# Performance work log

Hardware: AMD Instinct MI355X
Metric: run time of the kernel (lower is better)

Reference implementation:

```python
import jax, jax.numpy as jnp
import numpy as np

N = 100000   # nodes
E = 1250000  # edges
IN = 64
HID = 64
OUT = 64


def setup_inputs() -> dict:
    key = jax.random.key(0)
    ks = jax.random.split(key, 8)
    x = jax.random.normal(ks[0], (N, IN), dtype=jnp.float32)
    edge_index = jax.random.randint(ks[1], (2, E), 0, N, dtype=jnp.int64)
    s_in = 1.0 / np.sqrt(IN)
    s_h = 1.0 / np.sqrt(HID)
    W1 = jax.random.normal(ks[2], (IN, HID), dtype=jnp.float32) * s_in
    b1 = jnp.zeros((HID,), dtype=jnp.float32)
    W2 = jax.random.normal(ks[3], (HID, HID), dtype=jnp.float32) * s_h
    b2 = jnp.zeros((HID,), dtype=jnp.float32)
    Wp = jax.random.normal(ks[4], (HID, OUT), dtype=jnp.float32) * s_h
    bp = jnp.zeros((OUT,), dtype=jnp.float32)
    return {"x": x, "edge_index": edge_index, "W1": W1, "b1": b1,
            "W2": W2, "b2": b2, "Wp": Wp, "bp": bp}


def _gcn_conv(h, W, b, src, dst, inv_sqrt_deg):
    # PyG GCNConv with add_self_loops: x' = D^{-1/2} (A+I) D^{-1/2} (h W) + b
    m = h @ W                                   # [N, F]
    norm = inv_sqrt_deg[src] * inv_sqrt_deg[dst]  # [E]
    agg = jax.ops.segment_sum(m[src] * norm[:, None], dst, num_segments=N)
    agg = agg + m * (inv_sqrt_deg * inv_sqrt_deg)[:, None]  # self-loop term (norm = 1/deg)
    return agg + b


def reference(x, edge_index, W1, b1, W2, b2, Wp, bp):
    src = edge_index[0]
    dst = edge_index[1]
    # degree with self-loops (edge weight 1)
    deg = jax.ops.segment_sum(jnp.ones((E,), dtype=x.dtype), dst, num_segments=N) + 1.0
    inv_sqrt_deg = jax.lax.rsqrt(deg)
    # dropout is identity in eval mode
    h = jax.nn.relu(_gcn_conv(x, W1, b1, src, dst, inv_sqrt_deg))
    h = jax.nn.relu(_gcn_conv(h, W2, b2, src, dst, inv_sqrt_deg))
    z = h @ Wp + bp                             # [N, OUT]
    return z
```

## Files before the change

kernel.cpp:

```cpp
#include <hip/hip_runtime.h>

#define F 64
#define NPART 256
#define CAP 8192

typedef unsigned short u16x8 __attribute__((ext_vector_type(8)));
typedef _Float16       f16x8 __attribute__((ext_vector_type(8)));
typedef float          f32x4 __attribute__((ext_vector_type(4)));

__device__ __forceinline__ float h2f(unsigned short u) {
    _Float16 h; __builtin_memcpy(&h, &u, 2); return (float)h;
}
__device__ __forceinline__ unsigned short f2h(float f) {
    _Float16 h = (_Float16)f; unsigned short u; __builtin_memcpy(&u, &h, 2); return u;
}


__global__ void k_binit(int* bbase) {
    bbase[threadIdx.x * 16] = threadIdx.x * CAP;
}

template<int EPT>
__global__ __launch_bounds__(256)
void k_binGemm1(const int* __restrict__ src, const int* __restrict__ dst,
                int* bbase, int2* staging,
                const float* __restrict__ x, const float* __restrict__ W1,
                unsigned short* __restrict__ mhA,
                int nE, int nN, int nBin, int nTiles)
{
    __shared__ int lcnt[NPART];
    __shared__ int lbase[NPART];
    __shared__ _Float16 Wt[64 * 72];
    const int t = threadIdx.x;

    if (blockIdx.x < nBin) {
        const int i0 = blockIdx.x * 256 * EPT;
        lcnt[t] = 0;
        __syncthreads();
        int es[EPT], ed[EPT], bk[EPT];
#pragma unroll
        for (int k = 0; k < EPT; ++k) {
            const int i = i0 + k * 256 + t;
            if (i < nE) {
                es[k] = src[i];
                ed[k] = dst[i];
                bk[k] = (int)(((long long)ed[k] * NPART) / nN);
                atomicAdd(&lcnt[bk[k]], 1);
            } else bk[k] = -1;
        }
        __syncthreads();
        lbase[t] = atomicAdd(&bbase[t * 16], lcnt[t]);
        lcnt[t] = 0;
        __syncthreads();
#pragma unroll
        for (int k = 0; k < EPT; ++k) {
            if (bk[k] >= 0) {
                const int r   = atomicAdd(&lcnt[bk[k]], 1);
                const int pos = lbase[bk[k]] + r;
                if (pos < (bk[k] + 1) * CAP)
                    staging[pos] = make_int2(es[k], ed[k]);
            }
        }
    } else {
#pragma unroll
        for (int i = 0; i < 16; ++i) {
            const int idx = i * 256 + t;
            Wt[(idx & 63) * 72 + (idx >> 6)] = (_Float16)W1[idx];
        }
        __syncthreads();
        const int w    = t >> 6;
        const int l    = t & 63;
        const int lr   = l & 15;
        const int lg   = l >> 4;
        const int tile = (blockIdx.x - nBin) * 4 + w;
        if (tile >= nTiles) return;

        f16x8 bf[2][4];
#pragma unroll
        for (int kt = 0; kt < 2; ++kt)
#pragma unroll
            for (int ct = 0; ct < 4; ++ct)
                bf[kt][ct] = *(const f16x8*)&Wt[(ct * 16 + lr) * 72 + kt * 32 + lg * 8];

        const float* rp = x + (size_t)(tile * 16 + lr) * F;
        f16x8 af[2];
#pragma unroll
        for (int kt = 0; kt < 2; ++kt) {
            const float4 v0 = *(const float4*)(rp + kt * 32 + lg * 8);
            const float4 v1 = *(const float4*)(rp + kt * 32 + lg * 8 + 4);
            f16x8 a;
            a[0] = (_Float16)v0.x; a[1] = (_Float16)v0.y;
            a[2] = (_Float16)v0.z; a[3] = (_Float16)v0.w;
            a[4] = (_Float16)v1.x; a[5] = (_Float16)v1.y;
            a[6] = (_Float16)v1.z; a[7] = (_Float16)v1.w;
            af[kt] = a;
        }

        f32x4 acc[4] = {{0.f,0.f,0.f,0.f},{0.f,0.f,0.f,0.f},{0.f,0.f,0.f,0.f},{0.f,0.f,0.f,0.f}};
#pragma unroll
        for (int kt = 0; kt < 2; ++kt)
#pragma unroll
            for (int ct = 0; ct < 4; ++ct)
                acc[ct] = __builtin_amdgcn_mfma_f32_16x16x32_f16(af[kt], bf[kt][ct], acc[ct], 0, 0, 0);

        const int rowb = tile * 16 + lg * 4;
#pragma unroll
        for (int ct = 0; ct < 4; ++ct) {
            const int c = ct * 16 + lr;
#pragma unroll
            for (int r = 0; r < 4; ++r)
                mhA[(size_t)(rowb + r) * F + c] = f2h(acc[ct][r]);
        }
    }
}

__global__ __launch_bounds__(256)
void k_sortP(const int2* __restrict__ staging, const int* __restrict__ bbase,
             int* __restrict__ ebs, int* __restrict__ rowptr,
             float* __restrict__ isd, unsigned short* __restrict__ mhA,
             int nN, int nE) {
    __shared__ int pc[NPART];
    __shared__ int pcv[NPART];
    __shared__ int cnt[512];
    __shared__ int cur[512];
    const int p = blockIdx.x;
    const int t = threadIdx.x;

    int cval = bbase[t * 16] - t * CAP;
    if (cval > CAP) cval = CAP;
    if (cval < 0)   cval = 0;
    pc[t]  = cval;
    pcv[t] = cval;
    __syncthreads();
#pragma unroll
    for (int off = 1; off < NPART; off <<= 1) {
        const int a = (t >= off) ? pc[t - off] : 0;
        __syncthreads();
        pc[t] += a;
        __syncthreads();
    }
    const int cg    = pcv[p];
    const int ebase = pc[p] - cg;
    const int lo    = (int)(((long long)nN * p + NPART - 1) / NPART);
    const int hi    = (int)(((long long)nN * (p + 1) + NPART - 1) / NPART);
    const int npn   = hi - lo;

    cnt[t] = 0; cnt[t + 256] = 0;
    __syncthreads();
    const int2* st = staging + (size_t)p * CAP;
    for (int j = t; j < cg; j += 256) atomicAdd(&cnt[st[j].y - lo], 1);
    __syncthreads();

    const int c0 = cnt[t], c1 = cnt[t + 256];
#pragma unroll
    for (int off = 1; off < 512; off <<= 1) {
        const int a0 = (t >= off) ? cnt[t - off] : 0;
        const int a1 = (t + 256 >= off) ? cnt[t + 256 - off] : 0;
        __syncthreads();
        cnt[t] += a0; cnt[t + 256] += a1;
        __syncthreads();
    }
    const int e0 = cnt[t] - c0, e1 = cnt[t + 256] - c1;
    cur[t] = e0; cur[t + 256] = e1;

    if (t < npn)        { rowptr[lo + t]        = ebase + e0; isd[lo + t]        = rsqrtf((float)c0 + 1.0f); }
    if (t + 256 < npn)  { rowptr[lo + t + 256]  = ebase + e1; isd[lo + t + 256]  = rsqrtf((float)c1 + 1.0f); }
    if (p == NPART - 1 && t == 0) rowptr[nN] = ebase + cg;
    __syncthreads();

    for (int j = t; j < cg; j += 256) {
        const int2 e = st[j];
        const int  r = atomicAdd(&cur[e.y - lo], 1);
        ebs[ebase + r] = e.x;
    }

    for (int r = t; r < npn; r += 256) {
        const int row = lo + r;
        const float s = rsqrtf((float)((r < 256 ? c0 : 0) + 0) + 1.0f);
        (void)s;
        const float sr = isd[row];
        u16x8* rp = (u16x8*)(mhA + (size_t)row * F);
#pragma unroll
        for (int q = 0; q < 8; ++q) {
            u16x8 v = rp[q];
            u16x8 o;
#pragma unroll
            for (int j = 0; j < 8; ++j) o[j] = f2h(h2f(v[j]) * sr);
            rp[q] = o;
        }
    }
}


template<bool PROJ>
__global__ __launch_bounds__(256)
void k_aggGemm(const unsigned short* __restrict__ mhIn,
               const float* __restrict__ isd,
               const int* __restrict__ rowptr, const int* __restrict__ ebs,
               const float* __restrict__ W, const float* __restrict__ bin,
               const float* __restrict__ bout,
               unsigned short* __restrict__ outh, float* __restrict__ outf,
               int nN)
{
    __shared__ _Float16 Wt[64 * 72];
    __shared__ _Float16 A[32 * 72];
    const int t = threadIdx.x;
#pragma unroll
    for (int i = 0; i < 16; ++i) {
        const int idx = i * 256 + t;
        Wt[(idx & 63) * 72 + (idx >> 6)] = (_Float16)W[idx];
    }

    const int w  = t >> 6;
    const int l  = t & 63;
    const int nb = blockIdx.x * 32;
    const float bl = bin[l];

#pragma unroll
    for (int i = 0; i < 8; ++i) {
        const int n = nb + w * 8 + i;
        const int beg = __builtin_amdgcn_readfirstlane(rowptr[n]);
        const int end = __builtin_amdgcn_readfirstlane(rowptr[n + 1]);
        const float di = isd[n];
        float a0 = h2f(mhIn[(size_t)n * F + l]);
        float a1 = 0.f, a2 = 0.f, a3 = 0.f;
        int e = beg;
        for (; e + 8 <= end; e += 8) {
            const int s0 = ebs[e + 0], s1 = ebs[e + 1], s2 = ebs[e + 2], s3 = ebs[e + 3];
            const int s4 = ebs[e + 4], s5 = ebs[e + 5], s6 = ebs[e + 6], s7 = ebs[e + 7];
            const float v0 = h2f(mhIn[(size_t)s0 * F + l]);
            const float v1 = h2f(mhIn[(size_t)s1 * F + l]);
            const float v2 = h2f(mhIn[(size_t)s2 * F + l]);
            const float v3 = h2f(mhIn[(size_t)s3 * F + l]);
            const float v4 = h2f(mhIn[(size_t)s4 * F + l]);
            const float v5 = h2f(mhIn[(size_t)s5 * F + l]);
            const float v6 = h2f(mhIn[(size_t)s6 * F + l]);
            const float v7 = h2f(mhIn[(size_t)s7 * F + l]);
            a0 += v0; a1 += v1; a2 += v2; a3 += v3;
            a0 += v4; a1 += v5; a2 += v6; a3 += v7;
        }
        for (; e + 2 <= end; e += 2) {
            const int s0 = ebs[e + 0], s1 = ebs[e + 1];
            a0 += h2f(mhIn[(size_t)s0 * F + l]);
            a1 += h2f(mhIn[(size_t)s1 * F + l]);
        }
        if (e < end) a2 += h2f(mhIn[(size_t)ebs[e] * F + l]);
        const float v = ((a0 + a1) + (a2 + a3)) * di;
        A[(w * 8 + i) * 72 + l] = (_Float16)fmaxf(v + bl, 0.f);
    }
    __syncthreads();

    const int lr = l & 15;
    const int lg = l >> 4;
    const int th = w >> 1;
    const int ch = (w & 1) * 2;

    f16x8 bf[2][2];
#pragma unroll
    for (int kt = 0; kt < 2; ++kt)
#pragma unroll
        for (int ct = 0; ct < 2; ++ct)
            bf[kt][ct] = *(const f16x8*)&Wt[((ch + ct) * 16 + lr) * 72 + kt * 32 + lg * 8];

    f16x8 af[2];
#pragma unroll
    for (int kt = 0; kt < 2; ++kt)
        af[kt] = *(const f16x8*)&A[(th * 16 + lr) * 72 + kt * 32 + lg * 8];

    f32x4 acc[2] = {{0.f,0.f,0.f,0.f},{0.f,0.f,0.f,0.f}};
#pragma unroll
    for (int kt = 0; kt < 2; ++kt)
#pragma unroll
        for (int ct = 0; ct < 2; ++ct)
            acc[ct] = __builtin_amdgcn_mfma_f32_16x16x32_f16(af[kt], bf[kt][ct], acc[ct], 0, 0, 0);

    const int rowb = nb + th * 16 + lg * 4;
    float4 sc4;
    if (!PROJ) sc4 = *(const float4*)&isd[rowb];
    const float scv[4] = {sc4.x, sc4.y, sc4.z, sc4.w};
#pragma unroll
    for (int ct = 0; ct < 2; ++ct) {
        const int c = (ch + ct) * 16 + lr;
        float badd = 0.f;
        if (PROJ) badd = bout[c];
#pragma unroll
        for (int r = 0; r < 4; ++r) {
            if (PROJ) outf[(size_t)(rowb + r) * F + c] = acc[ct][r] + badd;
            else      outh[(size_t)(rowb + r) * F + c] = f2h(acc[ct][r] * scv[r]);
        }
    }
}


extern "C" void kernel_launch(void* const* d_in, const int* in_sizes, int n_in,
                              void* d_out, int out_size, void* d_ws, size_t ws_size,
                              hipStream_t stream)
{
    const float* x   = (const float*)d_in[0];
    const int*   ei  = (const int*)d_in[1];
    const float* W1  = (const float*)d_in[2];
    const float* b1  = (const float*)d_in[3];
    const float* W2  = (const float*)d_in[4];
    const float* b2  = (const float*)d_in[5];
    const float* Wp  = (const float*)d_in[6];
    const float* bp  = (const float*)d_in[7];
    float*       z   = (float*)d_out;

    const int nN = in_sizes[0] / F;
    const int nE = in_sizes[1] / 2;
    const int* srcp = ei;
    const int* dstp = ei + nE;

    char* ws = (char*)d_ws;
    size_t o = 0;
    auto alloc = [&](size_t bytes) { char* p = ws + o; o += (bytes + 255) & ~(size_t)255; return p; };
    float* isd    = (float*)alloc((size_t)nN * 4);
    int*   rowptr = (int*)  alloc(((size_t)nN + 1) * 4);
    int*   bbase  = (int*)  alloc((size_t)NPART * 16 * 4);
    int*   ebs    = (int*)  alloc((size_t)nE * 4);
    char*  U      = alloc((size_t)NPART * CAP * 8);
    int2*  staging = (int2*)U;
    unsigned short* mhB = (unsigned short*)U;
    unsigned short* mhA = (unsigned short*)alloc((size_t)nN * F * 2);

    constexpr int EPT = 16;
    const int gbB    = (nE + 256 * EPT - 1) / (256 * EPT);
    const int nTiles = nN / 16;
    const int gbG    = (nTiles + 3) / 4;
    const int gbF    = (nN + 31) / 32;

    k_binit<<<1, NPART, 0, stream>>>(bbase);
    k_binGemm1<EPT><<<gbB + gbG, 256, 0, stream>>>(srcp, dstp, bbase, staging,
                                                   x, W1, mhA, nE, nN, gbB, nTiles);
    k_sortP<<<NPART, 256, 0, stream>>>(staging, bbase, ebs, rowptr, isd, mhA, nN, nE);

    k_aggGemm<false><<<gbF, 256, 0, stream>>>(mhA, isd, rowptr, ebs, W2, b1, nullptr,
                                              mhB, nullptr, nN);
    k_aggGemm<true><<<gbF, 256, 0, stream>>>(mhB, isd, rowptr, ebs, Wp, b2, bp,
                                             nullptr, z, nN);
}
```

Before: 129.6 us.

## Split each wavefront across four edges with 8-byte vector gathers in aggregation

```diff
diff --git a/kernel.cpp b/kernel.cpp
--- a/kernel.cpp
+++ b/kernel.cpp
@@ -5,7 +5,9 @@
 #define CAP 8192
 
 typedef unsigned short u16x8 __attribute__((ext_vector_type(8)));
+typedef unsigned short u16x4 __attribute__((ext_vector_type(4)));
 typedef _Float16       f16x8 __attribute__((ext_vector_type(8)));
+typedef _Float16       f16x4 __attribute__((ext_vector_type(4)));
 typedef float          f32x4 __attribute__((ext_vector_type(4)));
 
 __device__ __forceinline__ float h2f(unsigned short u) {
@@ -176,8 +178,6 @@
 
     for (int r = t; r < npn; r += 256) {
         const int row = lo + r;
-        const float s = rsqrtf((float)((r < 256 ? c0 : 0) + 0) + 1.0f);
-        (void)s;
         const float sr = isd[row];
         u16x8* rp = (u16x8*)(mhA + (size_t)row * F);
 #pragma unroll
@@ -213,8 +213,10 @@
 
     const int w  = t >> 6;
     const int l  = t & 63;
+    const int q  = l >> 4;
+    const int r  = l & 15;
     const int nb = blockIdx.x * 32;
-    const float bl = bin[l];
+    const float4 bb = *(const float4*)(bin + r * 4);
 
 #pragma unroll
     for (int i = 0; i < 8; ++i) {
@@ -222,31 +224,51 @@
         const int beg = __builtin_amdgcn_readfirstlane(rowptr[n]);
         const int end = __builtin_amdgcn_readfirstlane(rowptr[n + 1]);
         const float di = isd[n];
-        float a0 = h2f(mhIn[(size_t)n * F + l]);
-        float a1 = 0.f, a2 = 0.f, a3 = 0.f;
+        float a0 = 0.f, a1 = 0.f, a2 = 0.f, a3 = 0.f;
+        float b0 = 0.f, b1 = 0.f, b2 = 0.f, b3 = 0.f;
+        if (q == 0) {
+            const u16x4 sv = *(const u16x4*)(mhIn + (size_t)n * F + r * 4);
+            a0 = h2f(sv[0]); a1 = h2f(sv[1]); a2 = h2f(sv[2]); a3 = h2f(sv[3]);
+        }
         int e = beg;
-        for (; e + 8 <= end; e += 8) {
-            const int s0 = ebs[e + 0], s1 = ebs[e + 1], s2 = ebs[e + 2], s3 = ebs[e + 3];
-            const int s4 = ebs[e + 4], s5 = ebs[e + 5], s6 = ebs[e + 6], s7 = ebs[e + 7];
-            const float v0 = h2f(mhIn[(size_t)s0 * F + l]);
-            const float v1 = h2f(mhIn[(size_t)s1 * F + l]);
-            const float v2 = h2f(mhIn[(size_t)s2 * F + l]);
-            const float v3 = h2f(mhIn[(size_t)s3 * F + l]);
-            const float v4 = h2f(mhIn[(size_t)s4 * F + l]);
-            const float v5 = h2f(mhIn[(size_t)s5 * F + l]);
-            const float v6 = h2f(mhIn[(size_t)s6 * F + l]);
-            const float v7 = h2f(mhIn[(size_t)s7 * F + l]);
-            a0 += v0; a1 += v1; a2 += v2; a3 += v3;
-            a0 += v4; a1 += v5; a2 += v6; a3 += v7;
-        }
-        for (; e + 2 <= end; e += 2) {
-            const int s0 = ebs[e + 0], s1 = ebs[e + 1];
-            a0 += h2f(mhIn[(size_t)s0 * F + l]);
-            a1 += h2f(mhIn[(size_t)s1 * F + l]);
-        }
-        if (e < end) a2 += h2f(mhIn[(size_t)ebs[e] * F + l]);
-        const float v = ((a0 + a1) + (a2 + a3)) * di;
-        A[(w * 8 + i) * 72 + l] = (_Float16)fmaxf(v + bl, 0.f);
+        for (; e + 16 <= end; e += 16) {
+            const int s0 = ebs[e + q];
+            const int s1 = ebs[e + 4 + q];
+            const int s2 = ebs[e + 8 + q];
+            const int s3 = ebs[e + 12 + q];
+            const u16x4 v0 = *(const u16x4*)(mhIn + (size_t)s0 * F + r * 4);
+            const u16x4 v1 = *(const u16x4*)(mhIn + (size_t)s1 * F + r * 4);
+            const u16x4 v2 = *(const u16x4*)(mhIn + (size_t)s2 * F + r * 4);
+            const u16x4 v3 = *(const u16x4*)(mhIn + (size_t)s3 * F + r * 4);
+            a0 += h2f(v0[0]); a1 += h2f(v0[1]); a2 += h2f(v0[2]); a3 += h2f(v0[3]);
+            b0 += h2f(v1[0]); b1 += h2f(v1[1]); b2 += h2f(v1[2]); b3 += h2f(v1[3]);
+            a0 += h2f(v2[0]); a1 += h2f(v2[1]); a2 += h2f(v2[2]); a3 += h2f(v2[3]);
+            b0 += h2f(v3[0]); b1 += h2f(v3[1]); b2 += h2f(v3[2]); b3 += h2f(v3[3]);
+        }
+        for (; e < end; e += 4) {
+            const int idx = e + q;
+            const int sc  = (idx < end) ? idx : end - 1;
+            const int s0  = ebs[sc];
+            const u16x4 v0 = *(const u16x4*)(mhIn + (size_t)s0 * F + r * 4);
+            const float msk = (idx < end) ? 1.f : 0.f;
+            b0 = fmaf(msk, h2f(v0[0]), b0);
+            b1 = fmaf(msk, h2f(v0[1]), b1);
+            b2 = fmaf(msk, h2f(v0[2]), b2);
+            b3 = fmaf(msk, h2f(v0[3]), b3);
+        }
+        a0 += b0; a1 += b1; a2 += b2; a3 += b3;
+        a0 += __shfl_xor(a0, 16); a1 += __shfl_xor(a1, 16);
+        a2 += __shfl_xor(a2, 16); a3 += __shfl_xor(a3, 16);
+        a0 += __shfl_xor(a0, 32); a1 += __shfl_xor(a1, 32);
+        a2 += __shfl_xor(a2, 32); a3 += __shfl_xor(a3, 32);
+        if (q == 0) {
+            f16x4 o;
+            o[0] = (_Float16)fmaxf(fmaf(a0, di, bb.x), 0.f);
+            o[1] = (_Float16)fmaxf(fmaf(a1, di, bb.y), 0.f);
+            o[2] = (_Float16)fmaxf(fmaf(a2, di, bb.z), 0.f);
+            o[3] = (_Float16)fmaxf(fmaf(a3, di, bb.w), 0.f);
+            *(f16x4*)&A[(w * 8 + i) * 72 + r * 4] = o;
+        }
     }
     __syncthreads();
 
@@ -275,7 +297,7 @@
             acc[ct] = __builtin_amdgcn_mfma_f32_16x16x32_f16(af[kt], bf[kt][ct], acc[ct], 0, 0, 0);
 
     const int rowb = nb + th * 16 + lg * 4;
-    float4 sc4;
+    float4 sc4 = {0.f, 0.f, 0.f, 0.f};
     if (!PROJ) sc4 = *(const float4*)&isd[rowb];
     const float scv[4] = {sc4.x, sc4.y, sc4.z, sc4.w};
 #pragma unroll
@@ -284,9 +306,9 @@
         float badd = 0.f;
         if (PROJ) badd = bout[c];
 #pragma unroll
-        for (int r = 0; r < 4; ++r) {
-            if (PROJ) outf[(size_t)(rowb + r) * F + c] = acc[ct][r] + badd;
-            else      outh[(size_t)(rowb + r) * F + c] = f2h(acc[ct][r] * scv[r]);
+        for (int rr = 0; rr < 4; ++rr) {
+            if (PROJ) outf[(size_t)(rowb + rr) * F + c] = acc[ct][rr] + badd;
+            else      outh[(size_t)(rowb + rr) * F + c] = f2h(acc[ct][rr] * scv[rr]);
         }
     }
 }
```

Measured after the change: 157.7 us. 21.7% more time.

## Interleave gathers across four rows with masked steps for more memory parallelism

Applied to the files above, without the earlier changes.

```diff
diff --git a/kernel.cpp b/kernel.cpp
--- a/kernel.cpp
+++ b/kernel.cpp
@@ -176,8 +176,6 @@
 
     for (int r = t; r < npn; r += 256) {
         const int row = lo + r;
-        const float s = rsqrtf((float)((r < 256 ? c0 : 0) + 0) + 1.0f);
-        (void)s;
         const float sr = isd[row];
         u16x8* rp = (u16x8*)(mhA + (size_t)row * F);
 #pragma unroll
@@ -189,6 +187,15 @@
             rp[q] = o;
         }
     }
+}
+
+__device__ __forceinline__ void gstep(const unsigned short* __restrict__ mh,
+                                      const int* __restrict__ ebs,
+                                      int ix, int en, int l, float& acc) {
+    int cl = (ix < en) ? ix : en - 1;
+    cl = (cl < 0) ? 0 : cl;
+    const float mk = (ix < en) ? 1.f : 0.f;
+    acc = fmaf(mk, h2f(mh[(size_t)ebs[cl] * F + l]), acc);
 }
 
 
@@ -217,36 +224,43 @@
     const float bl = bin[l];
 
 #pragma unroll
-    for (int i = 0; i < 8; ++i) {
-        const int n = nb + w * 8 + i;
-        const int beg = __builtin_amdgcn_readfirstlane(rowptr[n]);
-        const int end = __builtin_amdgcn_readfirstlane(rowptr[n + 1]);
-        const float di = isd[n];
-        float a0 = h2f(mhIn[(size_t)n * F + l]);
-        float a1 = 0.f, a2 = 0.f, a3 = 0.f;
-        int e = beg;
-        for (; e + 8 <= end; e += 8) {
-            const int s0 = ebs[e + 0], s1 = ebs[e + 1], s2 = ebs[e + 2], s3 = ebs[e + 3];
-            const int s4 = ebs[e + 4], s5 = ebs[e + 5], s6 = ebs[e + 6], s7 = ebs[e + 7];
-            const float v0 = h2f(mhIn[(size_t)s0 * F + l]);
-            const float v1 = h2f(mhIn[(size_t)s1 * F + l]);
-            const float v2 = h2f(mhIn[(size_t)s2 * F + l]);
-            const float v3 = h2f(mhIn[(size_t)s3 * F + l]);
-            const float v4 = h2f(mhIn[(size_t)s4 * F + l]);
-            const float v5 = h2f(mhIn[(size_t)s5 * F + l]);
-            const float v6 = h2f(mhIn[(size_t)s6 * F + l]);
-            const float v7 = h2f(mhIn[(size_t)s7 * F + l]);
-            a0 += v0; a1 += v1; a2 += v2; a3 += v3;
-            a0 += v4; a1 += v5; a2 += v6; a3 += v7;
-        }
-        for (; e + 2 <= end; e += 2) {
-            const int s0 = ebs[e + 0], s1 = ebs[e + 1];
-            a0 += h2f(mhIn[(size_t)s0 * F + l]);
-            a1 += h2f(mhIn[(size_t)s1 * F + l]);
-        }
-        if (e < end) a2 += h2f(mhIn[(size_t)ebs[e] * F + l]);
-        const float v = ((a0 + a1) + (a2 + a3)) * di;
-        A[(w * 8 + i) * 72 + l] = (_Float16)fmaxf(v + bl, 0.f);
+    for (int g = 0; g < 2; ++g) {
+        const int n0 = nb + w * 8 + g * 4;
+        const int b0 = __builtin_amdgcn_readfirstlane(rowptr[n0 + 0]);
+        const int e0 = __builtin_amdgcn_readfirstlane(rowptr[n0 + 1]);
+        const int e1 = __builtin_amdgcn_readfirstlane(rowptr[n0 + 2]);
+        const int e2 = __builtin_amdgcn_readfirstlane(rowptr[n0 + 3]);
+        const int e3 = __builtin_amdgcn_readfirstlane(rowptr[n0 + 4]);
+        const int b1 = e0, b2 = e1, b3 = e2;
+
+        const float di0 = isd[n0 + 0], di1 = isd[n0 + 1];
+        const float di2 = isd[n0 + 2], di3 = isd[n0 + 3];
+        float ac0 = h2f(mhIn[(size_t)(n0 + 0) * F + l]);
+        float ac1 = h2f(mhIn[(size_t)(n0 + 1) * F + l]);
+        float ac2 = h2f(mhIn[(size_t)(n0 + 2) * F + l]);
+        float ac3 = h2f(mhIn[(size_t)(n0 + 3) * F + l]);
+
+        const int d0 = e0 - b0, d1 = e1 - b1, d2 = e2 - b2, d3 = e3 - b3;
+        int mx = d0 > d1 ? d0 : d1;
+        if (d2 > mx) mx = d2;
+        if (d3 > mx) mx = d3;
+
+        for (int k = 0; k < mx; k += 4) {
+#pragma unroll
+            for (int j = 0; j < 4; ++j) gstep(mhIn, ebs, b0 + k + j, e0, l, ac0);
+#pragma unroll
+            for (int j = 0; j < 4; ++j) gstep(mhIn, ebs, b1 + k + j, e1, l, ac1);
+#pragma unroll
+            for (int j = 0; j < 4; ++j) gstep(mhIn, ebs, b2 + k + j, e2, l, ac2);
+#pragma unroll
+            for (int j = 0; j < 4; ++j) gstep(mhIn, ebs, b3 + k + j, e3, l, ac3);
+        }
+
+        _Float16* Ar = &A[(w * 8 + g * 4) * 72 + l];
+        Ar[0 * 72] = (_Float16)fmaxf(fmaf(ac0, di0, bl), 0.f);
+        Ar[1 * 72] = (_Float16)fmaxf(fmaf(ac1, di1, bl), 0.f);
+        Ar[2 * 72] = (_Float16)fmaxf(fmaf(ac2, di2, bl), 0.f);
+        Ar[3 * 72] = (_Float16)fmaxf(fmaf(ac3, di3, bl), 0.f);
     }
     __syncthreads();
 
@@ -275,7 +289,7 @@
             acc[ct] = __builtin_amdgcn_mfma_f32_16x16x32_f16(af[kt], bf[kt][ct], acc[ct], 0, 0, 0);
 
     const int rowb = nb + th * 16 + lg * 4;
-    float4 sc4;
+    float4 sc4 = {0.f, 0.f, 0.f, 0.f};
     if (!PROJ) sc4 = *(const float4*)&isd[rowb];
     const float scv[4] = {sc4.x, sc4.y, sc4.z, sc4.w};
 #pragma unroll
@@ -284,9 +298,9 @@
         float badd = 0.f;
         if (PROJ) badd = bout[c];
 #pragma unroll
-        for (int r = 0; r < 4; ++r) {
-            if (PROJ) outf[(size_t)(rowb + r) * F + c] = acc[ct][r] + badd;
-            else      outh[(size_t)(rowb + r) * F + c] = f2h(acc[ct][r] * scv[r]);
+        for (int rr = 0; rr < 4; ++rr) {
+            if (PROJ) outf[(size_t)(rowb + rr) * F + c] = acc[ct][rr] + badd;
+            else      outh[(size_t)(rowb + rr) * F + c] = f2h(acc[ct][rr] * scv[rr]);
         }
     }
 }
```

Result: slower. 146.3 us (+12.9%).

## Gather two edges per wavefront with half-precision pairs and shuffle-reduce

Applied to the files above, without the earlier changes.

```diff
diff --git a/kernel.cpp b/kernel.cpp
--- a/kernel.cpp
+++ b/kernel.cpp
@@ -6,6 +6,7 @@
 
 typedef unsigned short u16x8 __attribute__((ext_vector_type(8)));
 typedef _Float16       f16x8 __attribute__((ext_vector_type(8)));
+typedef _Float16       f16x2 __attribute__((ext_vector_type(2)));
 typedef float          f32x4 __attribute__((ext_vector_type(4)));
 
 __device__ __forceinline__ float h2f(unsigned short u) {
@@ -15,10 +16,6 @@
     _Float16 h = (_Float16)f; unsigned short u; __builtin_memcpy(&u, &h, 2); return u;
 }
 
-
-__global__ void k_binit(int* bbase) {
-    bbase[threadIdx.x * 16] = threadIdx.x * CAP;
-}
 
 template<int EPT>
 __global__ __launch_bounds__(256)
@@ -49,7 +46,7 @@
             } else bk[k] = -1;
         }
         __syncthreads();
-        lbase[t] = atomicAdd(&bbase[t * 16], lcnt[t]);
+        lbase[t] = t * CAP + atomicAdd(&bbase[t * 16], lcnt[t]);
         lcnt[t] = 0;
         __syncthreads();
 #pragma unroll
@@ -126,7 +123,7 @@
     const int p = blockIdx.x;
     const int t = threadIdx.x;
 
-    int cval = bbase[t * 16] - t * CAP;
+    int cval = bbase[t * 16];
     if (cval > CAP) cval = CAP;
     if (cval < 0)   cval = 0;
     pc[t]  = cval;
@@ -176,8 +173,6 @@
 
     for (int r = t; r < npn; r += 256) {
         const int row = lo + r;
-        const float s = rsqrtf((float)((r < 256 ? c0 : 0) + 0) + 1.0f);
-        (void)s;
         const float sr = isd[row];
         u16x8* rp = (u16x8*)(mhA + (size_t)row * F);
 #pragma unroll
@@ -189,6 +184,15 @@
             rp[q] = o;
         }
     }
+}
+
+__device__ __forceinline__ void g2(const unsigned short* __restrict__ mh,
+                                   int sLo, int sHi, int hl, int j2,
+                                   float& a0, float& a1) {
+    const int row = hl ? sHi : sLo;
+    const f16x2 v = *(const f16x2*)(mh + (size_t)row * F + j2);
+    a0 += (float)v[0];
+    a1 += (float)v[1];
 }
 
 
@@ -211,10 +215,13 @@
         Wt[(idx & 63) * 72 + (idx >> 6)] = (_Float16)W[idx];
     }
 
-    const int w  = t >> 6;
-    const int l  = t & 63;
-    const int nb = blockIdx.x * 32;
-    const float bl = bin[l];
+    const int w   = t >> 6;
+    const int l   = t & 63;
+    const int hl  = l >> 5;
+    const int j2  = (l & 31) * 2;
+    const int nb  = blockIdx.x * 32;
+    const float hsel = (hl == 0) ? 1.f : 0.f;
+    const float2 bb  = *(const float2*)(bin + j2);
 
 #pragma unroll
     for (int i = 0; i < 8; ++i) {
@@ -222,31 +229,36 @@
         const int beg = __builtin_amdgcn_readfirstlane(rowptr[n]);
         const int end = __builtin_amdgcn_readfirstlane(rowptr[n + 1]);
         const float di = isd[n];
-        float a0 = h2f(mhIn[(size_t)n * F + l]);
-        float a1 = 0.f, a2 = 0.f, a3 = 0.f;
+        const f16x2 sv = *(const f16x2*)(mhIn + (size_t)n * F + j2);
+        float a0 = hsel * (float)sv[0];
+        float a1 = hsel * (float)sv[1];
         int e = beg;
         for (; e + 8 <= end; e += 8) {
             const int s0 = ebs[e + 0], s1 = ebs[e + 1], s2 = ebs[e + 2], s3 = ebs[e + 3];
             const int s4 = ebs[e + 4], s5 = ebs[e + 5], s6 = ebs[e + 6], s7 = ebs[e + 7];
-            const float v0 = h2f(mhIn[(size_t)s0 * F + l]);
-            const float v1 = h2f(mhIn[(size_t)s1 * F + l]);
-            const float v2 = h2f(mhIn[(size_t)s2 * F + l]);
-            const float v3 = h2f(mhIn[(size_t)s3 * F + l]);
-            const float v4 = h2f(mhIn[(size_t)s4 * F + l]);
-            const float v5 = h2f(mhIn[(size_t)s5 * F + l]);
-            const float v6 = h2f(mhIn[(size_t)s6 * F + l]);
-            const float v7 = h2f(mhIn[(size_t)s7 * F + l]);
-            a0 += v0; a1 += v1; a2 += v2; a3 += v3;
-            a0 += v4; a1 += v5; a2 += v6; a3 += v7;
+            g2(mhIn, s0, s1, hl, j2, a0, a1);
+            g2(mhIn, s2, s3, hl, j2, a0, a1);
+            g2(mhIn, s4, s5, hl, j2, a0, a1);
+            g2(mhIn, s6, s7, hl, j2, a0, a1);
         }
         for (; e + 2 <= end; e += 2) {
             const int s0 = ebs[e + 0], s1 = ebs[e + 1];
-            a0 += h2f(mhIn[(size_t)s0 * F + l]);
-            a1 += h2f(mhIn[(size_t)s1 * F + l]);
-        }
-        if (e < end) a2 += h2f(mhIn[(size_t)ebs[e] * F + l]);
-        const float v = ((a0 + a1) + (a2 + a3)) * di;
-        A[(w * 8 + i) * 72 + l] = (_Float16)fmaxf(v + bl, 0.f);
+            g2(mhIn, s0, s1, hl, j2, a0, a1);
+        }
+        if (e < end) {
+            const int s0 = ebs[e];
+            const f16x2 v = *(const f16x2*)(mhIn + (size_t)s0 * F + j2);
+            a0 = fmaf(hsel, (float)v[0], a0);
+            a1 = fmaf(hsel, (float)v[1], a1);
+        }
+        a0 += __shfl_xor(a0, 32);
+        a1 += __shfl_xor(a1, 32);
+        if (hl == 0) {
+            f16x2 o;
+            o[0] = (_Float16)fmaxf(fmaf(a0, di, bb.x), 0.f);
+            o[1] = (_Float16)fmaxf(fmaf(a1, di, bb.y), 0.f);
+            *(f16x2*)&A[(w * 8 + i) * 72 + j2] = o;
+        }
     }
     __syncthreads();
 
@@ -275,7 +287,7 @@
             acc[ct] = __builtin_amdgcn_mfma_f32_16x16x32_f16(af[kt], bf[kt][ct], acc[ct], 0, 0, 0);
 
     const int rowb = nb + th * 16 + lg * 4;
-    float4 sc4;
+    float4 sc4 = {0.f, 0.f, 0.f, 0.f};
     if (!PROJ) sc4 = *(const float4*)&isd[rowb];
     const float scv[4] = {sc4.x, sc4.y, sc4.z, sc4.w};
 #pragma unroll
@@ -284,9 +296,9 @@
         float badd = 0.f;
         if (PROJ) badd = bout[c];
 #pragma unroll
-        for (int r = 0; r < 4; ++r) {
-            if (PROJ) outf[(size_t)(rowb + r) * F + c] = acc[ct][r] + badd;
-            else      outh[(size_t)(rowb + r) * F + c] = f2h(acc[ct][r] * scv[r]);
+        for (int rr = 0; rr < 4; ++rr) {
+            if (PROJ) outf[(size_t)(rowb + rr) * F + c] = acc[ct][rr] + badd;
+            else      outh[(size_t)(rowb + rr) * F + c] = f2h(acc[ct][rr] * scv[rr]);
         }
     }
 }
@@ -329,7 +341,7 @@
     const int gbG    = (nTiles + 3) / 4;
     const int gbF    = (nN + 31) / 32;
 
-    k_binit<<<1, NPART, 0, stream>>>(bbase);
+    hipMemsetAsync(bbase, 0, (size_t)NPART * 16 * 4, stream);
     k_binGemm1<EPT><<<gbB + gbG, 256, 0, stream>>>(srcp, dstp, bbase, staging,
                                                    x, W1, mhA, nE, nN, gbB, nTiles);
     k_sortP<<<NPART, 256, 0, stream>>>(staging, bbase, ebs, rowptr, isd, mhA, nN, nE);
```

Result: no change. 129.9 us (+0.2%).
